# Optimization experiments

Measured on AMD Instinct MI355X. Metric: run time of the kernel, lower is better.

## Reference

```python
import jax, jax.numpy as jnp
import numpy as np

QW_MAX = 127  # 2**(8-1) - 1


def setup_inputs() -> dict:
    key = jax.random.key(0)
    k1, k2, k3, k4, k5 = jax.random.split(key, 5)
    B, Din, H, Dout = 4096, 1024, 4096, 1024
    x = jax.random.normal(k1, (B, Din), dtype=jnp.float32)
    # float master weights (already transposed, as in quantify_weights: weight.T)
    w1f = jax.random.normal(k2, (Din, H), dtype=jnp.float32) * 0.02
    b1f = jax.random.normal(k3, (H,), dtype=jnp.float32) * 0.02
    w2f = jax.random.normal(k4, (H, Dout), dtype=jnp.float32) * 0.02
    b2f = jax.random.normal(k5, (Dout,), dtype=jnp.float32) * 0.02
    return {"x": x, "w1f": w1f, "b1f": b1f, "w2f": w2f, "b2f": b2f}


def _quantify_pair(w, b):
    # joint max-abs scale over weight and bias (matches quantify(x, x2))
    max_v = jnp.maximum(jnp.max(jnp.abs(w)), jnp.max(jnp.abs(b)))
    scale = max_v / QW_MAX
    wq = jnp.round(w / scale).astype(jnp.int8)
    bq = jnp.round(b / scale).astype(jnp.int8)
    return wq, bq, scale


def _dot_product(q_a, q_b, scale_a, scale_b, target_scale):
    # int8 GEMM with int32 accumulation, then requantize to int16
    y0 = q_a.astype(jnp.int32) @ q_b.astype(jnp.int32)  # [M, N] int32
    scale = scale_a * scale_b / target_scale
    return jnp.round(y0 * scale).astype(jnp.int16)


def reference(x, w1f, b1f, w2f, b2f):
    # weight quantization (done once at init in torch, inlined here)
    w1, b1, s1 = _quantify_pair(w1f, b1f)
    w2, b2, s2 = _quantify_pair(w2f, b2f)
    # dynamic activation quantization
    x_scale = jnp.max(jnp.abs(x)) / QW_MAX
    x_q = jnp.round(x / x_scale).astype(jnp.int8)
    # layer 1: target_scale = s1, so effective multiplier is x_scale
    o1 = _dot_product(x_q, w1, x_scale, s1, s1) + b1.astype(jnp.int16)
    # layer 2: note torch passes scale_1 (not x_scale) here — faithful to source
    o2 = _dot_product(jnp.maximum(o1, 0), w2, s1, s2, s2) + b2.astype(jnp.int16)
    # dequantize
    return o2.astype(jnp.float32) * s2
```

## Files before the change

kernel.cpp:

```cpp
#include <hip/hip_runtime.h>
#include <stdint.h>

typedef int   i32x4 __attribute__((ext_vector_type(4)));
typedef float f32x4 __attribute__((ext_vector_type(4)));

#define WS_PART    0
#define WS_XQ      32768
#define WS_W1QT    (WS_XQ   + 4096*1024)
#define WS_W2QT    (WS_W1QT + 4096*1024)
#define WS_PS      (WS_W2QT + 4096*1024)
#define WS_PH      (WS_PS   + 4096*4096)

__device__ __forceinline__ void async16(const void* g, void* l) {
  __builtin_amdgcn_global_load_lds(
      (const __attribute__((address_space(1))) unsigned*)g,
      (__attribute__((address_space(3))) unsigned*)l, 16, 0, 0);
}

__device__ __forceinline__ float block_absmax(const float* __restrict__ p0, int n0,
                                              const float* __restrict__ p1, int n1,
                                              float* red, float* slot) {
  int tid = threadIdx.x, nt = blockDim.x;
  float m = 0.f;
  for (int i = tid; i < n0; i += nt) m = fmaxf(m, fabsf(p0[i]));
  if (p1) for (int i = tid; i < n1; i += nt) m = fmaxf(m, fabsf(p1[i]));
  for (int off = 32; off; off >>= 1) m = fmaxf(m, __shfl_down(m, off));
  if ((tid & 63) == 0) red[tid >> 6] = m;
  __syncthreads();
  if (tid == 0) {
    int nw = nt >> 6;
    float M = red[0];
    for (int w = 1; w < nw; w++) M = fmaxf(M, red[w]);
    *slot = M;
  }
  __syncthreads();
  return *slot;
}

__global__ void k_absmax3(const float* __restrict__ x, const float* __restrict__ w1,
                          const float* __restrict__ w2, float* __restrict__ part) {
  int seg = blockIdx.x >> 9;
  int b = blockIdx.x & 511;
  const float* p = (seg == 0) ? x : (seg == 1) ? w1 : w2;
  int i = b * 256 + threadIdx.x;
  float m = 0.f;
  #pragma unroll
  for (int it = 0; it < 8; it++) {
    f32x4 v = ((const f32x4*)p)[i + it * 131072];
    m = fmaxf(m, fmaxf(fmaxf(fabsf(v.x), fabsf(v.y)), fmaxf(fabsf(v.z), fabsf(v.w))));
  }
  for (int off = 32; off; off >>= 1) m = fmaxf(m, __shfl_down(m, off));
  __shared__ float red[4];
  if ((threadIdx.x & 63) == 0) red[threadIdx.x >> 6] = m;
  __syncthreads();
  if (threadIdx.x == 0)
    part[blockIdx.x] = fmaxf(fmaxf(red[0], red[1]), fmaxf(red[2], red[3]));
}

__device__ __forceinline__ void quantT_body(const float* __restrict__ w, float s,
                                            i32x4* __restrict__ out, int C, int tkbits,
                                            int b) {
  int L = b * 256 + threadIdx.x;
  int h_in = L & 127;
  int kb = (L >> 7) & 3;
  int tk = (L >> 9) & ((1 << tkbits) - 1);
  int hblk = L >> (9 + tkbits);
  int h = hblk * 128 + h_in;
  int k0 = (tk * 4 + kb) * 16;
  int wd[4];
  #pragma unroll
  for (int d = 0; d < 4; d++) {
    unsigned acc = 0;
    #pragma unroll
    for (int j = 0; j < 4; j++) {
      float v = w[(size_t)(k0 + d * 4 + j) * C + h];
      int q = (int)rintf(v / s) & 255;
      acc |= (unsigned)q << (8 * j);
    }
    wd[d] = (int)acc;
  }
  i32x4 o; o.x = wd[0]; o.y = wd[1]; o.z = wd[2]; o.w = wd[3];
  out[L] = o;
}

__global__ void k_prep(const float* __restrict__ x, const float* __restrict__ w1f,
                       const float* __restrict__ w2f, const float* __restrict__ b1f,
                       const float* __restrict__ b2f, const float* __restrict__ part,
                       float* __restrict__ scales,
                       i32x4* __restrict__ xq, i32x4* __restrict__ w1qt,
                       i32x4* __restrict__ w2qt) {
  __shared__ float red[4];
  __shared__ float slot;
  int seg = blockIdx.x >> 10;
  int b = blockIdx.x & 1023;
  if (seg == 0) {
    float s = block_absmax(part, 512, nullptr, 0, red, &slot) / 127.0f;
    if (b == 0 && threadIdx.x == 0) scales[0] = s;
    int L = b * 256 + threadIdx.x;
    int m_in = L & 127, kb = (L >> 7) & 3, tk = (L >> 9) & 15, mblk = L >> 13;
    int m = mblk * 128 + m_in;
    int k0 = (tk * 4 + kb) * 16;
    const f32x4* px = (const f32x4*)(x + m * 1024 + k0);
    int wd[4];
    #pragma unroll
    for (int d = 0; d < 4; d++) {
      f32x4 v = px[d];
      int b0 = (int)rintf(v.x / s) & 255;
      int b1 = (int)rintf(v.y / s) & 255;
      int b2 = (int)rintf(v.z / s) & 255;
      int b3 = (int)rintf(v.w / s) & 255;
      wd[d] = b0 | (b1 << 8) | (b2 << 16) | (b3 << 24);
    }
    i32x4 o; o.x = wd[0]; o.y = wd[1]; o.z = wd[2]; o.w = wd[3];
    xq[L] = o;
  } else if (seg == 1) {
    float s = block_absmax(part + 512, 512, b1f, 4096, red, &slot) / 127.0f;
    if (b == 0 && threadIdx.x == 0) scales[1] = s;
    quantT_body(w1f, s, w1qt, 4096, 4, b);
  } else {
    float s = block_absmax(part + 1024, 512, b2f, 1024, red, &slot) / 127.0f;
    if (b == 0 && threadIdx.x == 0) scales[2] = s;
    quantT_body(w2f, s, w2qt, 1024, 6, b);
  }
}

__launch_bounds__(512, 4)
__global__ void k_gemm1(const i32x4* __restrict__ Aq, const i32x4* __restrict__ Bq,
                        const float* __restrict__ scales, const float* __restrict__ b1f,
                        unsigned* __restrict__ plane_s, unsigned* __restrict__ plane_h) {
  __shared__ i32x4 st[2048];

  int tid = threadIdx.x;
  int L = blockIdx.x;
  int wg = (L & 7) * 256 + (L >> 3);
  int T  = wg & 63;
  int bb = wg >> 6;
  int half = T & 1, hblk = T >> 1;
  int wid = tid >> 6, lane = tid & 63;
  int kh = wid >> 2, w2 = wid & 3;
  int wm = w2 & 1, wn = w2 >> 1;
  int g = lane >> 4, l15 = lane & 15;
  int t256 = tid & 255;
  int sbase = kh * 512;
  int a_src = (t256 >> 6) * 128 + half * 64 + (t256 & 63);
  int b_idx = g * 128 + wn * 64 + l15;

  const i32x4* gA = Aq + (size_t)hblk * 8192;
  const i32x4* gB = Bq + (size_t)bb * 8192;

  async16(gA + (size_t)(kh * 8) * 512 + a_src, &st[sbase + t256]);
  i32x4 bf[4];
  {
    const i32x4* pB = gB + (size_t)(kh * 8) * 512;
    #pragma unroll
    for (int c = 0; c < 4; c++) bf[c] = pB[b_idx + c * 16];
  }

  float sx  = scales[0];
  float s1v = scales[1];
  float mult1 = sx * s1v / s1v;

  i32x4 acc[2][4];
  #pragma unroll
  for (int r = 0; r < 2; r++)
    #pragma unroll
    for (int c = 0; c < 4; c++) acc[r][c] = (i32x4)(0);

  int aoff = g * 64 + wm * 32 + l15;

  __syncthreads();

  for (int tt = 0; tt < 8; ++tt) {
    int cur = tt & 1;
    if (tt + 1 < 8) {
      async16(gA + (size_t)(kh * 8 + tt + 1) * 512 + a_src,
              &st[sbase + (cur ^ 1) * 256 + t256]);
      __builtin_amdgcn_sched_barrier(0);
    }
    i32x4 af[2];
    #pragma unroll
    for (int r = 0; r < 2; r++) af[r] = st[sbase + cur * 256 + aoff + r * 16];
    #pragma unroll
    for (int r = 0; r < 2; r++)
      #pragma unroll
      for (int c = 0; c < 4; c++)
        acc[r][c] = __builtin_amdgcn_mfma_i32_16x16x64_i8(af[r], bf[c], acc[r][c], 0, 0, 0);
    if (tt + 1 < 8) {
      __builtin_amdgcn_sched_barrier(0);
      const i32x4* pB = gB + (size_t)(kh * 8 + tt + 1) * 512;
      #pragma unroll
      for (int c = 0; c < 4; c++) bf[c] = pB[b_idx + c * 16];
      asm volatile("s_waitcnt vmcnt(4)" ::: "memory");
      __builtin_amdgcn_s_barrier();
      __builtin_amdgcn_sched_barrier(0);
    }
  }

  __syncthreads();
  int* mg = (int*)st;
  if (kh == 1) {
    #pragma unroll
    for (int r = 0; r < 2; r++)
      #pragma unroll
      for (int c = 0; c < 4; c++)
        #pragma unroll
        for (int q = 0; q < 4; q++)
          mg[((r * 4 + c) * 4 + q) * 256 + t256] = acc[r][c][q];
  }
  __syncthreads();
  if (kh == 0) {
    #pragma unroll
    for (int r = 0; r < 2; r++) {
      int rg = wm * 2 + r;
      int hbase = T * 64 + wm * 32 + r * 16 + 4 * g;
      int bq0 = (int)rintf(b1f[hbase + 0] / s1v);
      int bq1 = (int)rintf(b1f[hbase + 1] / s1v);
      int bq2 = (int)rintf(b1f[hbase + 2] / s1v);
      int bq3 = (int)rintf(b1f[hbase + 3] / s1v);
      #pragma unroll
      for (int c = 0; c < 4; c++) {
        unsigned lo = 0, hi = 0;
        #pragma unroll
        for (int q = 0; q < 4; q++) {
          int y0 = acc[r][c][q] + mg[((r * 4 + c) * 4 + q) * 256 + t256];
          int bqv = (q == 0) ? bq0 : (q == 1) ? bq1 : (q == 2) ? bq2 : bq3;
          int o = (short)((int)rintf((float)y0 * mult1) + bqv);
          int a = o > 0 ? o : 0;
          int s8 = (int)(signed char)(a & 0xFF);
          int h8 = (a >> 8) + (s8 < 0 ? 1 : 0);
          lo |= (unsigned)(s8 & 0xFF) << (8 * q);
          hi |= (unsigned)(h8 & 0xFF) << (8 * q);
        }
        int m_in = wn * 64 + c * 16 + l15;
        unsigned idx = (((unsigned)(bb * 64 + T) * 512u + (unsigned)(rg * 128 + m_in)) << 2) + g;
        plane_s[idx] = lo;
        plane_h[idx] = hi;
      }
    }
  }
}

__launch_bounds__(512, 4)
__global__ void k_gemm2(const i32x4* __restrict__ Ps, const i32x4* __restrict__ Ph,
                        const i32x4* __restrict__ Bq, const float* __restrict__ scales,
                        const float* __restrict__ b2f, float* __restrict__ out) {
  __shared__ i32x4 st[2048];

  int tid = threadIdx.x;
  int L = blockIdx.x;
  int mb = ((L & 7) << 3) | ((L >> 3) & 7);
  int nb = L >> 6;
  int mblk = mb >> 1, half = mb & 1;
  int wid = tid >> 6, lane = tid & 63;
  int kh = wid >> 2, w2 = wid & 3;
  int wm = w2 & 1, wn = w2 >> 1;
  int g = lane >> 4, l15 = lane & 15;
  int t256 = tid & 255;
  int sbase = kh * 1024;
  int a_idx = (t256 >> 6) * 128 + half * 64 + (t256 & 63);
  int b_idx = g * 128 + wn * 64 + l15;

  {
    int t = kh * 32;
    const i32x4* pS = Ps + ((size_t)(mblk * 64 + t) << 9);
    const i32x4* pH = Ph + ((size_t)(mblk * 64 + t) << 9);
    async16(pS + a_idx, &st[sbase + t256]);
    async16(pH + a_idx, &st[sbase + 256 + t256]);
  }
  i32x4 bf[4];
  {
    const i32x4* pB = Bq + ((size_t)(nb * 64 + kh * 32) << 9);
    #pragma unroll
    for (int c = 0; c < 4; c++) bf[c] = pB[b_idx + c * 16];
  }

  float s1v = scales[1];
  float s2v = scales[2];
  float mult2 = s1v * s2v / s2v;
  int bq[4];
  #pragma unroll
  for (int c = 0; c < 4; c++)
    bq[c] = (int)rintf(b2f[nb * 128 + wn * 64 + c * 16 + l15] / s2v);

  i32x4 accS[2][4], accH[2][4];
  #pragma unroll
  for (int r = 0; r < 2; r++)
    #pragma unroll
    for (int c = 0; c < 4; c++) { accS[r][c] = (i32x4)(0); accH[r][c] = (i32x4)(0); }

  __syncthreads();

  for (int tt = 0; tt < 32; ++tt) {
    int cur = tt & 1;
    if (tt + 1 < 32) {
      int t = kh * 32 + tt + 1;
      const i32x4* pS = Ps + ((size_t)(mblk * 64 + t) << 9);
      const i32x4* pH = Ph + ((size_t)(mblk * 64 + t) << 9);
      int R1 = sbase + (cur ^ 1) * 512;
      async16(pS + a_idx, &st[R1 + t256]);
      async16(pH + a_idx, &st[R1 + 256 + t256]);
      __builtin_amdgcn_sched_barrier(0);
    }
    int R = sbase + cur * 512;
    i32x4 aS[2], aH[2];
    #pragma unroll
    for (int r = 0; r < 2; r++) {
      aS[r] = st[R + g * 64 + wm * 32 + r * 16 + l15];
      aH[r] = st[R + 256 + g * 64 + wm * 32 + r * 16 + l15];
    }
    #pragma unroll
    for (int r = 0; r < 2; r++)
      #pragma unroll
      for (int c = 0; c < 4; c++) {
        accS[r][c] = __builtin_amdgcn_mfma_i32_16x16x64_i8(aS[r], bf[c], accS[r][c], 0, 0, 0);
        accH[r][c] = __builtin_amdgcn_mfma_i32_16x16x64_i8(aH[r], bf[c], accH[r][c], 0, 0, 0);
      }
    if (tt + 1 < 32) {
      __builtin_amdgcn_sched_barrier(0);
      const i32x4* pB = Bq + ((size_t)(nb * 64 + kh * 32 + tt + 1) << 9);
      #pragma unroll
      for (int c = 0; c < 4; c++) bf[c] = pB[b_idx + c * 16];
      asm volatile("s_waitcnt vmcnt(4)" ::: "memory");
      __builtin_amdgcn_s_barrier();
      __builtin_amdgcn_sched_barrier(0);
    }
  }

  int y0p[2][4][4];
  #pragma unroll
  for (int r = 0; r < 2; r++)
    #pragma unroll
    for (int c = 0; c < 4; c++)
      #pragma unroll
      for (int q = 0; q < 4; q++)
        y0p[r][c][q] = accS[r][c][q] + accH[r][c][q] * 256;

  __syncthreads();
  int* mg = (int*)st;
  if (kh == 1) {
    #pragma unroll
    for (int r = 0; r < 2; r++)
      #pragma unroll
      for (int c = 0; c < 4; c++)
        #pragma unroll
        for (int q = 0; q < 4; q++)
          mg[((r * 4 + c) * 4 + q) * 256 + t256] = y0p[r][c][q];
  }
  __syncthreads();
  if (kh == 0) {
    #pragma unroll
    for (int r = 0; r < 2; r++) {
      int m0 = mb * 64 + wm * 32 + r * 16 + 4 * g;
      #pragma unroll
      for (int c = 0; c < 4; c++) {
        int n = nb * 128 + wn * 64 + c * 16 + l15;
        #pragma unroll
        for (int q = 0; q < 4; q++) {
          int y0 = y0p[r][c][q] + mg[((r * 4 + c) * 4 + q) * 256 + t256];
          int o = (short)((int)rintf((float)y0 * mult2) + bq[c]);
          out[(size_t)(m0 + q) * 1024 + n] = (float)o * s2v;
        }
      }
    }
  }
}

extern "C" void kernel_launch(void* const* d_in, const int* in_sizes, int n_in,
                              void* d_out, int out_size, void* d_ws, size_t ws_size,
                              hipStream_t stream) {
  const float* x   = (const float*)d_in[0];
  const float* w1f = (const float*)d_in[1];
  const float* b1f = (const float*)d_in[2];
  const float* w2f = (const float*)d_in[3];
  const float* b2f = (const float*)d_in[4];
  float* out = (float*)d_out;

  char* ws = (char*)d_ws;
  float*  part    = (float*)(ws + WS_PART);
  float*  scales  = part + 1536;
  i32x4*  xq      = (i32x4*)(ws + WS_XQ);
  i32x4*  w1qt    = (i32x4*)(ws + WS_W1QT);
  i32x4*  w2qt    = (i32x4*)(ws + WS_W2QT);
  unsigned* ps    = (unsigned*)(ws + WS_PS);
  unsigned* ph    = (unsigned*)(ws + WS_PH);

  k_absmax3<<<1536, 256, 0, stream>>>(x, w1f, w2f, part);
  k_prep<<<3072, 256, 0, stream>>>(x, w1f, w2f, b1f, b2f, part, scales, xq, w1qt, w2qt);
  k_gemm1<<<2048, 512, 0, stream>>>(w1qt, xq, scales, b1f, ps, ph);
  k_gemm2<<<512, 512, 0, stream>>>((const i32x4*)ps, (const i32x4*)ph, w2qt,
                                   scales, b2f, out);
}
```

Before: 180.8 us.

## Preload all A tiles into LDS and double-buffer B fragments in registers

Replaces the double-buffered LDS ring for the A operand in k_gemm1 with a single upfront async load of all 8 K-steps into a doubled LDS buffer. This removes the per-iteration barrier and waitcnt. B fragments are now prefetched two steps ahead with a register double buffer, and the loop is fully unrolled. The cost is twice the LDS per block (64KB) and more registers, which may lower occupancy under the 512x4 launch bounds. The whole A load must also land before the first MFMA can start.

Result: no change. 183.9 us (+1.7%).

```diff
diff --git a/kernel.cpp b/kernel.cpp
--- a/kernel.cpp
+++ b/kernel.cpp
@@ -128,7 +128,7 @@
 __global__ void k_gemm1(const i32x4* __restrict__ Aq, const i32x4* __restrict__ Bq,
                         const float* __restrict__ scales, const float* __restrict__ b1f,
                         unsigned* __restrict__ plane_s, unsigned* __restrict__ plane_h) {
-  __shared__ i32x4 st[2048];
+  __shared__ i32x4 st[4096];
 
   int tid = threadIdx.x;
   int L = blockIdx.x;
@@ -141,20 +141,16 @@
   int wm = w2 & 1, wn = w2 >> 1;
   int g = lane >> 4, l15 = lane & 15;
   int t256 = tid & 255;
-  int sbase = kh * 512;
   int a_src = (t256 >> 6) * 128 + half * 64 + (t256 & 63);
   int b_idx = g * 128 + wn * 64 + l15;
 
   const i32x4* gA = Aq + (size_t)hblk * 8192;
   const i32x4* gB = Bq + (size_t)bb * 8192;
 
-  async16(gA + (size_t)(kh * 8) * 512 + a_src, &st[sbase + t256]);
-  i32x4 bf[4];
-  {
-    const i32x4* pB = gB + (size_t)(kh * 8) * 512;
-    #pragma unroll
-    for (int c = 0; c < 4; c++) bf[c] = pB[b_idx + c * 16];
-  }
+  #pragma unroll
+  for (int tt = 0; tt < 8; ++tt)
+    async16(gA + (size_t)(kh * 8 + tt) * 512 + a_src,
+            &st[kh * 2048 + tt * 256 + t256]);
 
   float sx  = scales[0];
   float s1v = scales[1];
@@ -168,31 +164,30 @@
 
   int aoff = g * 64 + wm * 32 + l15;
 
-  __syncthreads();
-
+  i32x4 bf[4], bn[4];
+  #pragma unroll
+  for (int c = 0; c < 4; c++) bf[c] = gB[(size_t)(kh * 8) * 512 + b_idx + c * 16];
+  #pragma unroll
+  for (int c = 0; c < 4; c++) bn[c] = gB[(size_t)(kh * 8 + 1) * 512 + b_idx + c * 16];
+
+  __syncthreads();
+
+  #pragma unroll
   for (int tt = 0; tt < 8; ++tt) {
-    int cur = tt & 1;
-    if (tt + 1 < 8) {
-      async16(gA + (size_t)(kh * 8 + tt + 1) * 512 + a_src,
-              &st[sbase + (cur ^ 1) * 256 + t256]);
-      __builtin_amdgcn_sched_barrier(0);
-    }
     i32x4 af[2];
     #pragma unroll
-    for (int r = 0; r < 2; r++) af[r] = st[sbase + cur * 256 + aoff + r * 16];
+    for (int r = 0; r < 2; r++) af[r] = st[kh * 2048 + tt * 256 + aoff + r * 16];
     #pragma unroll
     for (int r = 0; r < 2; r++)
       #pragma unroll
       for (int c = 0; c < 4; c++)
         acc[r][c] = __builtin_amdgcn_mfma_i32_16x16x64_i8(af[r], bf[c], acc[r][c], 0, 0, 0);
-    if (tt + 1 < 8) {
-      __builtin_amdgcn_sched_barrier(0);
-      const i32x4* pB = gB + (size_t)(kh * 8 + tt + 1) * 512;
-      #pragma unroll
-      for (int c = 0; c < 4; c++) bf[c] = pB[b_idx + c * 16];
-      asm volatile("s_waitcnt vmcnt(4)" ::: "memory");
-      __builtin_amdgcn_s_barrier();
-      __builtin_amdgcn_sched_barrier(0);
+    #pragma unroll
+    for (int c = 0; c < 4; c++) bf[c] = bn[c];
+    if (tt + 2 < 8) {
+      const i32x4* pB = gB + (size_t)(kh * 8 + tt + 2) * 512;
+      #pragma unroll
+      for (int c = 0; c < 4; c++) bn[c] = pB[b_idx + c * 16];
     }
   }
 
```
